# Kernel tuning notes

Hardware: AMD Instinct MI355X
Metric: run time of the kernel (lower is better)

## Reference

```python
import jax, jax.numpy as jnp
import numpy as np

FORGET_BIAS = 1.0  # tf.nn.rnn_cell.LSTMCell default
HIDDEN = 64


def setup_inputs() -> dict:
    key = jax.random.key(0)
    k1, k2 = jax.random.split(key)
    B, T, D = 4096, 9, 512
    x = jax.random.normal(k1, (B, T, D), dtype=jnp.float32)
    # Fused LSTM kernel: [(D + H), 4H], gate order (i, j, f, o) as in TF LSTMCell
    kernel = jax.random.normal(k2, (D + HIDDEN, 4 * HIDDEN), dtype=jnp.float32) * 0.02
    bias = jnp.zeros((4 * HIDDEN,), dtype=jnp.float32)
    return {"x": x, "kernel": kernel, "bias": bias}


def _lstm_scan(x, kernel, bias):
    B, T, D = x.shape
    H = HIDDEN
    # Split kernel into input and recurrent parts for a cleaner scan body.
    Wx = kernel[:D]          # [D, 4H]
    Wh = kernel[D:]          # [H, 4H]
    # Precompute input contributions for all timesteps in one big GEMM.
    xg = jnp.einsum('btd,dg->btg', x, Wx) + bias  # [B, T, 4H]

    def step(carry, xg_t):
        c, h = carry
        gates = xg_t + h @ Wh  # [B, 4H]
        i, j, f, o = jnp.split(gates, 4, axis=-1)  # TF gate order: i, j, f, o
        c_new = jax.nn.sigmoid(f + FORGET_BIAS) * c + jax.nn.sigmoid(i) * jnp.tanh(j)
        h_new = jax.nn.sigmoid(o) * jnp.tanh(c_new)
        return (c_new, h_new), h_new

    c0 = jnp.zeros((B, H), dtype=x.dtype)
    h0 = jnp.zeros((B, H), dtype=x.dtype)
    _, hs = jax.lax.scan(step, (c0, h0), jnp.swapaxes(xg, 0, 1))  # hs: [T, B, H]
    return jnp.transpose(hs, (1, 0, 2))  # [B, T, H]


def reference(x, kernel, bias):
    return _lstm_scan(x, kernel, bias)
```

## Files before the change

kernel.cpp:

```cpp
#include <hip/hip_runtime.h>
#include <math.h>

#define T_STEPS 9
#define D_IN    512
#define HID     64
#define G4      256
#define BPB     8
#define ROWS    72
#define NCH     8

typedef short  short8 __attribute__((ext_vector_type(8)));
typedef float  f32x4  __attribute__((ext_vector_type(4)));
typedef unsigned int uint;
typedef unsigned short ushort;

__device__ __forceinline__ ushort f2bf(float f) {
    uint u = __float_as_uint(f);
    u = (u + 0x7FFFu + ((u >> 16) & 1u)) >> 16;
    return (ushort)u;
}
__device__ __forceinline__ float fsig(float x) {
    return 1.0f / (1.0f + __expf(-x));
}
__device__ __forceinline__ float ftanh(float x) {
    float t = __expf(-2.0f * fabsf(x));
    float r = (1.0f - t) / (1.0f + t);
    return copysignf(r, x);
}
__device__ __forceinline__ short8 cvt8(f32x4 lo, f32x4 hi) {
    union { uint u[4]; short8 s; } r;
    asm("v_cvt_pk_bf16_f32 %0, %1, %2" : "=v"(r.u[0]) : "v"(lo[0]), "v"(lo[1]));
    asm("v_cvt_pk_bf16_f32 %0, %1, %2" : "=v"(r.u[1]) : "v"(lo[2]), "v"(lo[3]));
    asm("v_cvt_pk_bf16_f32 %0, %1, %2" : "=v"(r.u[2]) : "v"(hi[0]), "v"(hi[1]));
    asm("v_cvt_pk_bf16_f32 %0, %1, %2" : "=v"(r.u[3]) : "v"(hi[2]), "v"(hi[3]));
    return r.s;
}
__device__ __forceinline__ void gl2lds16(const float* g, float* l) {
    __builtin_amdgcn_global_load_lds(
        (const __attribute__((address_space(1))) void*)g,
        (__attribute__((address_space(3))) void*)l, 16, 0, 0);
}

__global__ __launch_bounds__(256)
void prep_w(const float* __restrict__ kern, ushort* __restrict__ wxT,
            ushort* __restrict__ whT)
{
    const int blk = blockIdx.x;
    const int n   = threadIdx.x;
    const int krow0 = (blk < 64) ? blk * 8 : 512 + (blk - 64) * 8;
    union { ushort us[8]; short8 v; } o;
    #pragma unroll
    for (int j = 0; j < 8; ++j)
        o.us[j] = f2bf(kern[(size_t)(krow0 + j) * G4 + n]);
    if (blk < 64) *(short8*)&wxT[((size_t)blk * 256 + n) * 8] = o.v;
    else          *(short8*)&whT[((size_t)(blk - 64) * 256 + n) * 8] = o.v;
}

__global__ __launch_bounds__(256, 2)
void lstm_fused(const float* __restrict__ x, const ushort* __restrict__ wxT,
                const ushort* __restrict__ whT, const float* __restrict__ bias,
                float* __restrict__ out)
{
    __shared__ float  sX[3][80 * 64];
    __shared__ ushort sH[1024];

    const int t = threadIdx.x;
    const int w = t >> 6, l = t & 63;
    const int lane15 = l & 15, quad = l >> 4;
    const int u = w * 16 + lane15;

    const float* xbase = x + (size_t)blockIdx.x * (ROWS * D_IN);
    int soff[5];
    #pragma unroll
    for (int j = 0; j < 5; ++j) {
        int m   = w * 5 + j;
        int row = m * 4 + (l >> 4);
        int b_  = row & 7, s_ = row >> 3;
        int xr  = b_ * 9 + (s_ < 9 ? s_ : 8);
        int oct = ((l & 15) >> 1) ^ (row & 7);
        soff[j] = xr * 512 + oct * 8 + (l & 1) * 4;
    }

    #pragma unroll
    for (int j = 0; j < 5; ++j)
        gl2lds16(xbase + soff[j] + 0 * 64, &sX[0][(w * 5 + j) * 256]);
    __builtin_amdgcn_sched_barrier(0);
    #pragma unroll
    for (int j = 0; j < 5; ++j)
        gl2lds16(xbase + soff[j] + 1 * 64, &sX[1][(w * 5 + j) * 256]);
    __builtin_amdgcn_sched_barrier(0);

    if (t < 128) {
        uint4 z = {0u, 0u, 0u, 0u};
        *(uint4*)&sH[t * 8] = z;
    }
    asm volatile("s_waitcnt lgkmcnt(0)" ::: "memory");

    f32x4 acc[5][4];
    #pragma unroll
    for (int i = 0; i < 5; ++i)
        #pragma unroll
        for (int g = 0; g < 4; ++g)
            acc[i][g] = (f32x4){0.f, 0.f, 0.f, 0.f};

    short8 bFb[2][4];

    #pragma unroll
    for (int k = 0; k < NCH; ++k) {
        if (k < NCH - 1) asm volatile("s_waitcnt vmcnt(5)" ::: "memory");
        else             asm volatile("s_waitcnt vmcnt(0)" ::: "memory");
        __builtin_amdgcn_sched_barrier(0);
        __builtin_amdgcn_s_barrier();
        __builtin_amdgcn_sched_barrier(0);

        #pragma unroll
        for (int kk = 0; kk < 2; ++kk)
            #pragma unroll
            for (int g = 0; g < 4; ++g)
                bFb[kk][g] = *(const short8*)
                    &wxT[(size_t)(((k * 2 + kk) * 4 + quad) * 256 + g * 64 + u) * 8];
        __builtin_amdgcn_sched_barrier(0);

        if (k < NCH - 2) {
            float* dst = &sX[(k + 2) % 3][0];
            #pragma unroll
            for (int j = 0; j < 5; ++j)
                gl2lds16(xbase + soff[j] + (k + 2) * 64, dst + (w * 5 + j) * 256);
        }
        __builtin_amdgcn_sched_barrier(0);

        #pragma unroll
        for (int kk = 0; kk < 2; ++kk) {
            #pragma unroll
            for (int i = 0; i < 5; ++i) {
                int row = i * 16 + lane15;
                int op  = (((kk * 4 + quad) ^ (row & 7)) << 3);
                f32x4 lo = *(const f32x4*)&sX[k % 3][row * 64 + op];
                f32x4 hi = *(const f32x4*)&sX[k % 3][row * 64 + op + 4];
                short8 aF = cvt8(lo, hi);
                #pragma unroll
                for (int g = 0; g < 4; ++g)
                    acc[i][g] = __builtin_amdgcn_mfma_f32_16x16x32_bf16(
                        aF, bFb[kk][g], acc[i][g], 0, 0, 0);
            }
        }
    }

    short8 whF[4][2];
    #pragma unroll
    for (int g = 0; g < 4; ++g)
        #pragma unroll
        for (int kh = 0; kh < 2; ++kh)
            whF[g][kh] = *(const short8*)&whT[(size_t)((kh * 4 + quad) * 256 + g * 64 + u) * 8];

    float bia[4];
    bia[0] = bias[u];
    bia[1] = bias[64 + u];
    bia[2] = bias[128 + u] + 1.0f;
    bia[3] = bias[192 + u];

    float cst[4] = {0.f, 0.f, 0.f, 0.f};
    const int b0 = blockIdx.x * BPB;

    #pragma unroll
    for (int s = 0; s < T_STEPS; ++s) {
        const int  i = s >> 1;
        const int  p = s & 1;
        const bool active = ((quad >> 1) == p);
        const int  bofs = (quad & 1) * 4;

        f32x4 g4[4];
        #pragma unroll
        for (int g = 0; g < 4; ++g)
            #pragma unroll
            for (int r = 0; r < 4; ++r)
                g4[g][r] = acc[i][g][r] + bia[g];

        short8 aF[2];
        #pragma unroll
        for (int kh = 0; kh < 2; ++kh)
            aF[kh] = *(const short8*)&sH[((kh * 4 + quad) * 16 + lane15) * 8];

        #pragma unroll
        for (int g = 0; g < 4; ++g)
            #pragma unroll
            for (int kh = 0; kh < 2; ++kh)
                g4[g] = __builtin_amdgcn_mfma_f32_16x16x32_bf16(aF[kh], whF[g][kh], g4[g], 0, 0, 0);

        const int wrow = 8 * ((s + 1) & 1);
        #pragma unroll
        for (int r = 0; r < 4; ++r) {
            float cp = __shfl_xor(cst[r], 32);
            if (active) {
                float ii = fsig(g4[0][r]);
                float jj = ftanh(g4[1][r]);
                float ff = fsig(g4[2][r]);
                float oo = fsig(g4[3][r]);
                float c  = ff * cp + ii * jj;
                cst[r] = c;
                float h = oo * ftanh(c);
                int bb = bofs + r;
                out[((size_t)(b0 + bb) * T_STEPS + s) * HID + u] = h;
                sH[((u >> 3) * 16 + wrow + bb) * 8 + (u & 7)] = f2bf(h);
            }
        }
        asm volatile("s_waitcnt lgkmcnt(0)" ::: "memory");
        __builtin_amdgcn_sched_barrier(0);
        __builtin_amdgcn_s_barrier();
        __builtin_amdgcn_sched_barrier(0);
    }
}

extern "C" void kernel_launch(void* const* d_in, const int* in_sizes, int n_in,
                              void* d_out, int out_size, void* d_ws, size_t ws_size,
                              hipStream_t stream)
{
    const float* x    = (const float*)d_in[0];
    const float* kern = (const float*)d_in[1];
    const float* bias = (const float*)d_in[2];
    float* out = (float*)d_out;

    const int B = in_sizes[0] / (T_STEPS * D_IN);

    ushort* wxT = (ushort*)d_ws;
    ushort* whT = (ushort*)((char*)d_ws + 262144);

    prep_w<<<72, 256, 0, stream>>>(kern, wxT, whT);
    lstm_fused<<<B / BPB, 256, 0, stream>>>(x, wxT, whT, bias, out);
}
```

Measured before the change: 125.1 us.

## Stage x through registers as bf16 in LDS and double-buffer Wx fragments

Replaces the direct global-to-LDS fp32 copies of x with register loads that are converted to bf16 before being written to LDS. The MFMA loop can then read A fragments straight from LDS without a per-chunk conversion, and LDS traffic is halved. The Wx B-fragments are double-buffered and prefetched one chunk ahead, with x prefetched three chunks ahead in registers. This costs more VGPRs, which may reduce occupancy, and puts the conversion work and LDS stores on the critical path before each barrier.

```diff
diff --git a/kernel.cpp b/kernel.cpp
--- a/kernel.cpp
+++ b/kernel.cpp
@@ -6,7 +6,6 @@
 #define HID     64
 #define G4      256
 #define BPB     8
-#define ROWS    72
 #define NCH     8
 
 typedef short  short8 __attribute__((ext_vector_type(8)));
@@ -27,18 +26,10 @@
     float r = (1.0f - t) / (1.0f + t);
     return copysignf(r, x);
 }
-__device__ __forceinline__ short8 cvt8(f32x4 lo, f32x4 hi) {
-    union { uint u[4]; short8 s; } r;
-    asm("v_cvt_pk_bf16_f32 %0, %1, %2" : "=v"(r.u[0]) : "v"(lo[0]), "v"(lo[1]));
-    asm("v_cvt_pk_bf16_f32 %0, %1, %2" : "=v"(r.u[1]) : "v"(lo[2]), "v"(lo[3]));
-    asm("v_cvt_pk_bf16_f32 %0, %1, %2" : "=v"(r.u[2]) : "v"(hi[0]), "v"(hi[1]));
-    asm("v_cvt_pk_bf16_f32 %0, %1, %2" : "=v"(r.u[3]) : "v"(hi[2]), "v"(hi[3]));
-    return r.s;
-}
-__device__ __forceinline__ void gl2lds16(const float* g, float* l) {
-    __builtin_amdgcn_global_load_lds(
-        (const __attribute__((address_space(1))) void*)g,
-        (__attribute__((address_space(3))) void*)l, 16, 0, 0);
+__device__ __forceinline__ uint cvtpk(float a, float b) {
+    uint r;
+    asm("v_cvt_pk_bf16_f32 %0, %1, %2" : "=v"(r) : "v"(a), "v"(b));
+    return r;
 }
 
 __global__ __launch_bounds__(256)
@@ -61,40 +52,54 @@
                 const ushort* __restrict__ whT, const float* __restrict__ bias,
                 float* __restrict__ out)
 {
-    __shared__ float  sX[3][80 * 64];
-    __shared__ ushort sH[1024];
+    __shared__ __align__(16) ushort sA[3][80 * 64];
+    __shared__ __align__(16) ushort sH[1024];
 
     const int t = threadIdx.x;
     const int w = t >> 6, l = t & 63;
     const int lane15 = l & 15, quad = l >> 4;
     const int u = w * 16 + lane15;
 
-    const float* xbase = x + (size_t)blockIdx.x * (ROWS * D_IN);
-    int soff[5];
+    const float* xbase = x + (size_t)blockIdx.x * (72 * D_IN);
+    const int sq = t & 15, ow = sq >> 1, hw = sq & 1;
+    int src[5], wad[5];
     #pragma unroll
     for (int j = 0; j < 5; ++j) {
-        int m   = w * 5 + j;
-        int row = m * 4 + (l >> 4);
-        int b_  = row & 7, s_ = row >> 3;
-        int xr  = b_ * 9 + (s_ < 9 ? s_ : 8);
-        int oct = ((l & 15) >> 1) ^ (row & 7);
-        soff[j] = xr * 512 + oct * 8 + (l & 1) * 4;
-    }
-
-    #pragma unroll
-    for (int j = 0; j < 5; ++j)
-        gl2lds16(xbase + soff[j] + 0 * 64, &sX[0][(w * 5 + j) * 256]);
-    __builtin_amdgcn_sched_barrier(0);
-    #pragma unroll
-    for (int j = 0; j < 5; ++j)
-        gl2lds16(xbase + soff[j] + 1 * 64, &sX[1][(w * 5 + j) * 256]);
-    __builtin_amdgcn_sched_barrier(0);
+        int row = j * 16 + (t >> 4);
+        int b_ = row & 7, s_ = row >> 3;
+        if (s_ > 8) s_ = 8;
+        src[j] = (b_ * 9 + s_) * 512 + sq * 4;
+        wad[j] = row * 64 + ((ow ^ (row & 7)) << 3) + (hw << 2);
+    }
 
     if (t < 128) {
         uint4 z = {0u, 0u, 0u, 0u};
         *(uint4*)&sH[t * 8] = z;
     }
-    asm volatile("s_waitcnt lgkmcnt(0)" ::: "memory");
+
+    float4 svA[5], svB[5];
+    #pragma unroll
+    for (int j = 0; j < 5; ++j) svA[j] = *(const float4*)&xbase[src[j]];
+    #pragma unroll
+    for (int j = 0; j < 5; ++j) svB[j] = *(const float4*)&xbase[src[j] + 64];
+
+    short8 bFb[2][2][4];
+    #pragma unroll
+    for (int kk = 0; kk < 2; ++kk)
+        #pragma unroll
+        for (int g = 0; g < 4; ++g)
+            bFb[0][kk][g] = *(const short8*)
+                &wxT[(size_t)((kk * 4 + quad) * 256 + g * 64 + u) * 8];
+
+    #pragma unroll
+    for (int j = 0; j < 5; ++j) {
+        uint2 p;
+        p.x = cvtpk(svA[j].x, svA[j].y);
+        p.y = cvtpk(svA[j].z, svA[j].w);
+        *(uint2*)&sA[0][wad[j]] = p;
+    }
+    #pragma unroll
+    for (int j = 0; j < 5; ++j) svA[j] = *(const float4*)&xbase[src[j] + 128];
 
     f32x4 acc[5][4];
     #pragma unroll
@@ -103,45 +108,50 @@
         for (int g = 0; g < 4; ++g)
             acc[i][g] = (f32x4){0.f, 0.f, 0.f, 0.f};
 
-    short8 bFb[2][4];
-
     #pragma unroll
     for (int k = 0; k < NCH; ++k) {
-        if (k < NCH - 1) asm volatile("s_waitcnt vmcnt(5)" ::: "memory");
-        else             asm volatile("s_waitcnt vmcnt(0)" ::: "memory");
+        if (k < NCH - 1) {
+            #pragma unroll
+            for (int j = 0; j < 5; ++j) {
+                float4 v = ((k + 1) & 1) ? svB[j] : svA[j];
+                uint2 p;
+                p.x = cvtpk(v.x, v.y);
+                p.y = cvtpk(v.z, v.w);
+                *(uint2*)&sA[(k + 1) % 3][wad[j]] = p;
+            }
+        }
+        if (k < NCH - 1) {
+            #pragma unroll
+            for (int kk = 0; kk < 2; ++kk)
+                #pragma unroll
+                for (int g = 0; g < 4; ++g)
+                    bFb[(k + 1) & 1][kk][g] = *(const short8*)
+                        &wxT[(size_t)((((k + 1) * 2 + kk) * 4 + quad) * 256
+                                      + g * 64 + u) * 8];
+        }
+        if (k < NCH - 3) {
+            #pragma unroll
+            for (int j = 0; j < 5; ++j) {
+                float4 v = *(const float4*)&xbase[src[j] + (k + 3) * 64];
+                if ((k + 3) & 1) svB[j] = v; else svA[j] = v;
+            }
+        }
+        asm volatile("s_waitcnt lgkmcnt(0)" ::: "memory");
         __builtin_amdgcn_sched_barrier(0);
         __builtin_amdgcn_s_barrier();
         __builtin_amdgcn_sched_barrier(0);
-
-        #pragma unroll
-        for (int kk = 0; kk < 2; ++kk)
-            #pragma unroll
-            for (int g = 0; g < 4; ++g)
-                bFb[kk][g] = *(const short8*)
-                    &wxT[(size_t)(((k * 2 + kk) * 4 + quad) * 256 + g * 64 + u) * 8];
-        __builtin_amdgcn_sched_barrier(0);
-
-        if (k < NCH - 2) {
-            float* dst = &sX[(k + 2) % 3][0];
-            #pragma unroll
-            for (int j = 0; j < 5; ++j)
-                gl2lds16(xbase + soff[j] + (k + 2) * 64, dst + (w * 5 + j) * 256);
-        }
-        __builtin_amdgcn_sched_barrier(0);
-
+        asm volatile("" ::: "memory");
         #pragma unroll
         for (int kk = 0; kk < 2; ++kk) {
             #pragma unroll
             for (int i = 0; i < 5; ++i) {
                 int row = i * 16 + lane15;
-                int op  = (((kk * 4 + quad) ^ (row & 7)) << 3);
-                f32x4 lo = *(const f32x4*)&sX[k % 3][row * 64 + op];
-                f32x4 hi = *(const f32x4*)&sX[k % 3][row * 64 + op + 4];
-                short8 aF = cvt8(lo, hi);
+                short8 aF = *(const short8*)
+                    &sA[k % 3][row * 64 + (((kk * 4 + quad) ^ (row & 7)) << 3)];
                 #pragma unroll
                 for (int g = 0; g < 4; ++g)
                     acc[i][g] = __builtin_amdgcn_mfma_f32_16x16x32_bf16(
-                        aF, bFb[kk][g], acc[i][g], 0, 0, 0);
+                        aF, bFb[k & 1][kk][g], acc[i][g], 0, 0, 0);
             }
         }
     }
@@ -151,7 +161,8 @@
     for (int g = 0; g < 4; ++g)
         #pragma unroll
         for (int kh = 0; kh < 2; ++kh)
-            whF[g][kh] = *(const short8*)&whT[(size_t)((kh * 4 + quad) * 256 + g * 64 + u) * 8];
+            whF[g][kh] = *(const short8*)
+                &whT[(size_t)((kh * 4 + quad) * 256 + g * 64 + u) * 8];
 
     float bia[4];
     bia[0] = bias[u];
@@ -185,7 +196,8 @@
         for (int g = 0; g < 4; ++g)
             #pragma unroll
             for (int kh = 0; kh < 2; ++kh)
-                g4[g] = __builtin_amdgcn_mfma_f32_16x16x32_bf16(aF[kh], whF[g][kh], g4[g], 0, 0, 0);
+                g4[g] = __builtin_amdgcn_mfma_f32_16x16x32_bf16(
+                    aF[kh], whF[g][kh], g4[g], 0, 0, 0);
 
         const int wrow = 8 * ((s + 1) & 1);
         #pragma unroll
```

New measurement: 127.1 us. No clear change (+1.6%).
